# Optimization experiments

Measured on AMD Instinct MI355X. Metric: run time of the kernel, lower is better.

## Reference

```python
import jax, jax.numpy as jnp
import numpy as np

B, T, E, H = 2, 4096, 1024, 16
D = E // H  # head dim = 64

def setup_inputs() -> dict:
    key = jax.random.key(0)
    ks = jax.random.split(key, 5)
    x = jax.random.normal(ks[0], (B, T, E), dtype=jnp.float32)
    # torch Linear(n_embed, 3*n_embed): y = x @ W.T + b ; we store W already transposed as (E, 3E)
    w_qkv = jax.random.normal(ks[1], (E, 3 * E), dtype=jnp.float32) * (1.0 / np.sqrt(E))
    b_qkv = jax.random.normal(ks[2], (3 * E,), dtype=jnp.float32) * 0.02
    w_out = jax.random.normal(ks[3], (E, E), dtype=jnp.float32) * (1.0 / np.sqrt(E))
    b_out = jax.random.normal(ks[4], (E,), dtype=jnp.float32) * 0.02
    return {"x": x, "w_qkv": w_qkv, "b_qkv": b_qkv, "w_out": w_out, "b_out": b_out}

def reference(x, w_qkv, b_qkv, w_out, b_out):
    b, t, e = x.shape
    qkv = x @ w_qkv + b_qkv                      # (B,T,3E)
    # matches torch: view(B,T,H,3D) then chunk(3, dim=-1)
    qkv = qkv.reshape(b, t, H, 3 * D)
    q, k, v = jnp.split(qkv, 3, axis=-1)          # each (B,T,H,D)
    q = q.transpose(0, 2, 1, 3)                   # (B,H,T,D)
    k = k.transpose(0, 2, 1, 3)
    v = v.transpose(0, 2, 1, 3)
    scores = jnp.einsum('bhqd,bhkd->bhqk', q, k) / jnp.sqrt(jnp.float32(D))
    causal = jnp.tril(jnp.ones((t, t), dtype=bool))
    scores = jnp.where(causal, scores, jnp.float32(-jnp.inf))
    w = jax.nn.softmax(scores, axis=-1)           # (B,H,T,T)
    out = jnp.einsum('bhqk,bhkd->bhqd', w, v)     # (B,H,T,D)
    out = out.transpose(0, 2, 1, 3).reshape(b, t, e)
    return out @ w_out + b_out
```

## Files before the change

kernel.cpp:

```cpp
#include <hip/hip_runtime.h>
#include <stdint.h>
#include <math.h>

#define T_SEQ 4096

typedef __attribute__((ext_vector_type(8))) short short8;
typedef __attribute__((ext_vector_type(4))) float f32x4;
typedef __attribute__((ext_vector_type(16))) float f32x16;
typedef __attribute__((ext_vector_type(4))) uint16_t u16x4;

__device__ __forceinline__ uint16_t f2bf(float f) {
  uint32_t u = __float_as_uint(f);
  u += 0x7FFFu + ((u >> 16) & 1u);
  return (uint16_t)(u >> 16);
}

__device__ __forceinline__ void gload_lds16(const uint16_t* g, uint16_t* l) {
  __builtin_amdgcn_global_load_lds(
      (const __attribute__((address_space(1))) void*)g,
      (__attribute__((address_space(3))) void*)l, 16, 0, 0);
}

__global__ void __launch_bounds__(256) k_cvt(const float* __restrict__ in,
                                             uint16_t* __restrict__ out, int n4) {
  int i = blockIdx.x * 256 + threadIdx.x;
  if (i >= n4) return;
  float4 v = reinterpret_cast<const float4*>(in)[i];
  u16x4 o = { f2bf(v.x), f2bf(v.y), f2bf(v.z), f2bf(v.w) };
  reinterpret_cast<u16x4*>(out)[i] = o;
}

__global__ void __launch_bounds__(256) k_tc(const float* __restrict__ w,
                                            uint16_t* __restrict__ wt, int R, int C) {
  __shared__ uint16_t tile[32][33];
  int tx = threadIdx.x & 31, ty = threadIdx.x >> 5;
  int r0 = blockIdx.y * 32, c0 = blockIdx.x * 32;
#pragma unroll
  for (int i = 0; i < 4; i++)
    tile[ty + 8 * i][tx] = f2bf(w[(size_t)(r0 + ty + 8 * i) * C + c0 + tx]);
  __syncthreads();
#pragma unroll
  for (int i = 0; i < 4; i++)
    wt[(size_t)(c0 + ty + 8 * i) * R + r0 + tx] = tile[tx][ty + 8 * i];
}

__global__ void __launch_bounds__(256) k_vt(const uint16_t* __restrict__ qkv,
                                            uint16_t* __restrict__ vT) {
  __shared__ uint16_t tile[64][65];
  const int bh = blockIdx.y, b = bh >> 4, h = bh & 15;
  const int t0 = blockIdx.x * 64;
  const int tid = threadIdx.x;
  const int r = tid >> 3, c8 = tid & 7;
  const uint16_t* src = qkv + ((size_t)b * T_SEQ + t0) * 3072 + h * 192 + 128;
#pragma unroll
  for (int i = 0; i < 2; i++) {
    int row = r + 32 * i;
    short8 v = *reinterpret_cast<const short8*>(src + (size_t)row * 3072 + c8 * 8);
#pragma unroll
    for (int j = 0; j < 8; j++) tile[row][c8 * 8 + j] = (uint16_t)v[j];
  }
  __syncthreads();
  uint16_t* dst = vT + ((size_t)bh * 64) * T_SEQ + t0;
#pragma unroll
  for (int i = 0; i < 2; i++) {
    int d = r + 32 * i;
    short8 v;
#pragma unroll
    for (int j = 0; j < 8; j++) v[j] = (short)tile[c8 * 8 + j][d];
    *reinterpret_cast<short8*>(dst + (size_t)d * T_SEQ + c8 * 8) = v;
  }
}

template <int BF16_OUT>
__global__ void __launch_bounds__(256, 2) k_gemm(const uint16_t* __restrict__ A,
                                                 const uint16_t* __restrict__ BT,
                                                 const float* __restrict__ bias,
                                                 void* __restrict__ Cout,
                                                 int M, int N, int K) {
  __shared__ __align__(16) uint16_t As[2][128 * 64];
  __shared__ __align__(16) uint16_t Bs[2][128 * 64];
  const int tid = threadIdx.x;
  const int lane = tid & 63, wid = tid >> 6;
  const int lr = lane & 15, lg = lane >> 4;
  const int wr = wid >> 1, wc = wid & 1;

  const int bid = blockIdx.x;
  const int cpx = gridDim.x >> 3;
  const int lin = (bid & 7) * cpx + (bid >> 3);
  const int mt = M >> 7;
  const int n0 = (lin / mt) * 128;
  const int m0 = (lin % mt) * 128;

  const f32x4 vzero = {0.f, 0.f, 0.f, 0.f};
  f32x4 acc[4][4];
#pragma unroll
  for (int i = 0; i < 4; i++)
#pragma unroll
    for (int j = 0; j < 4; j++) acc[i][j] = vzero;

  const int sl = lane >> 3, ss = lane & 7;
  const int swzs = (ss ^ sl) * 8;
  const uint16_t* a0 = A + (size_t)(m0 + wid * 32 + sl) * K + swzs;
  const uint16_t* b0 = BT + (size_t)(n0 + wid * 32 + sl) * K + swzs;
  const size_t r8 = (size_t)8 * K;

#define STAGE(bsel, t)                                                   \
  do {                                                                   \
    const int koff_ = (t) * 64;                                          \
    gload_lds16(a0 + koff_,          &As[bsel][(wid * 32 + 0) * 64]);    \
    gload_lds16(a0 + r8 + koff_,     &As[bsel][(wid * 32 + 8) * 64]);    \
    gload_lds16(a0 + 2 * r8 + koff_, &As[bsel][(wid * 32 + 16) * 64]);   \
    gload_lds16(a0 + 3 * r8 + koff_, &As[bsel][(wid * 32 + 24) * 64]);   \
    gload_lds16(b0 + koff_,          &Bs[bsel][(wid * 32 + 0) * 64]);    \
    gload_lds16(b0 + r8 + koff_,     &Bs[bsel][(wid * 32 + 8) * 64]);    \
    gload_lds16(b0 + 2 * r8 + koff_, &Bs[bsel][(wid * 32 + 16) * 64]);   \
    gload_lds16(b0 + 3 * r8 + koff_, &Bs[bsel][(wid * 32 + 24) * 64]);   \
  } while (0)

  const int nt = K >> 6;
  const int fsw = lr & 7;
  STAGE(0, 0);
  STAGE(1, 1);
  __syncthreads();

  for (int t = 0; t < nt; ++t) {
    const int cur = t & 1;
#pragma unroll
    for (int ks = 0; ks < 2; ++ks) {
      const int col = (((ks * 4 + lg) ^ fsw) * 8);
      short8 af[4], bf[4];
#pragma unroll
      for (int mi = 0; mi < 4; ++mi)
        af[mi] = *reinterpret_cast<const short8*>(
            &As[cur][(wr * 64 + mi * 16 + lr) * 64 + col]);
#pragma unroll
      for (int nj = 0; nj < 4; ++nj)
        bf[nj] = *reinterpret_cast<const short8*>(
            &Bs[cur][(wc * 64 + nj * 16 + lr) * 64 + col]);
      __builtin_amdgcn_s_setprio(1);
#pragma unroll
      for (int mi = 0; mi < 4; ++mi)
#pragma unroll
        for (int nj = 0; nj < 4; ++nj)
          acc[mi][nj] = __builtin_amdgcn_mfma_f32_16x16x32_bf16(af[mi], bf[nj], acc[mi][nj], 0, 0, 0);
      __builtin_amdgcn_s_setprio(0);
    }
    __syncthreads();
    if (t + 2 < nt) STAGE(cur, t + 2);
  }
#undef STAGE

#pragma unroll
  for (int nj = 0; nj < 4; nj++) {
    int col = n0 + wc * 64 + nj * 16 + lr;
    float bv = bias[col];
#pragma unroll
    for (int mi = 0; mi < 4; mi++) {
      int rowb = m0 + wr * 64 + mi * 16 + lg * 4;
#pragma unroll
      for (int r = 0; r < 4; r++) {
        float v = acc[mi][nj][r] + bv;
        if (BF16_OUT)
          ((uint16_t*)Cout)[(size_t)(rowb + r) * N + col] = f2bf(v);
        else
          ((float*)Cout)[(size_t)(rowb + r) * N + col] = v;
      }
    }
  }
}

__global__ void __launch_bounds__(512, 2) k_gemm256(const uint16_t* __restrict__ A,
                                                    const uint16_t* __restrict__ BT,
                                                    const float* __restrict__ bias,
                                                    uint16_t* __restrict__ Cout,
                                                    int M, int N, int K) {
  __shared__ __align__(16) uint16_t As[2][256 * 32];
  __shared__ __align__(16) uint16_t Bs[2][256 * 32];
  const int tid = threadIdx.x;
  const int lane = tid & 63, wid = tid >> 6;
  const int lr = lane & 15, lg = lane >> 4;
  const int wr = wid >> 2, wc = wid & 3;

  const int bid = blockIdx.x;
  const int cpx = gridDim.x >> 3;
  const int lin = (bid & 7) * cpx + (bid >> 3);
  const int mt = M >> 8;
  const int n0 = (lin / mt) * 256;
  const int m0 = (lin % mt) * 256;

  const f32x4 vzero = {0.f, 0.f, 0.f, 0.f};
  f32x4 acc[8][4];
#pragma unroll
  for (int i = 0; i < 8; i++)
#pragma unroll
    for (int j = 0; j < 4; j++) acc[i][j] = vzero;

  const int row0 = tid >> 2;
  const int gc = (tid & 3) ^ ((tid >> 3) & 3);
  const uint16_t* a0 = A + (size_t)(m0 + row0) * K + gc * 8;
  const uint16_t* b0 = BT + (size_t)(n0 + row0) * K + gc * 8;
  const size_t rstep = (size_t)128 * K;

#define STAGE2(bsel, t)                                                    \
  do {                                                                     \
    const int ko_ = (t) * 32;                                              \
    gload_lds16(a0 + ko_,         &As[bsel][wid * 512]);                   \
    gload_lds16(a0 + rstep + ko_, &As[bsel][wid * 512 + 4096]);            \
    gload_lds16(b0 + ko_,         &Bs[bsel][wid * 512]);                   \
    gload_lds16(b0 + rstep + ko_, &Bs[bsel][wid * 512 + 4096]);            \
  } while (0)

  const int nt = K >> 5;
  const int fc = (lg ^ ((lr >> 1) & 3)) * 8;
  STAGE2(0, 0);
  STAGE2(1, 1);
  __syncthreads();

  for (int t = 0; t < nt; ++t) {
    const int cur = t & 1;
    short8 af[8], bf[4];
#pragma unroll
    for (int mi = 0; mi < 8; ++mi)
      af[mi] = *reinterpret_cast<const short8*>(
          &As[cur][(wr * 128 + mi * 16 + lr) * 32 + fc]);
#pragma unroll
    for (int nj = 0; nj < 4; ++nj)
      bf[nj] = *reinterpret_cast<const short8*>(
          &Bs[cur][(wc * 64 + nj * 16 + lr) * 32 + fc]);
    __builtin_amdgcn_s_setprio(1);
#pragma unroll
    for (int mi = 0; mi < 8; ++mi)
#pragma unroll
      for (int nj = 0; nj < 4; ++nj)
        acc[mi][nj] = __builtin_amdgcn_mfma_f32_16x16x32_bf16(af[mi], bf[nj], acc[mi][nj], 0, 0, 0);
    __builtin_amdgcn_s_setprio(0);
    __syncthreads();
    if (t + 2 < nt) STAGE2(cur, t + 2);
  }
#undef STAGE2

#pragma unroll
  for (int nj = 0; nj < 4; nj++) {
    int col = n0 + wc * 64 + nj * 16 + lr;
    float bv = bias[col];
#pragma unroll
    for (int mi = 0; mi < 8; mi++) {
      int rowb = m0 + wr * 128 + mi * 16 + lg * 4;
#pragma unroll
      for (int r = 0; r < 4; r++)
        Cout[(size_t)(rowb + r) * N + col] = f2bf(acc[mi][nj][r] + bv);
    }
  }
}

#define KVB 64
__global__ void __launch_bounds__(256) k_attn(const uint16_t* __restrict__ qkv,
                                              const uint16_t* __restrict__ vT,
                                              uint16_t* __restrict__ out) {
  __shared__ __align__(16) char lds[32768];
  const int tid = threadIdx.x;
  const int lane = tid & 63, wid = tid >> 6;
  const int l31 = lane & 31, hi = lane >> 5;
  const int hi4 = hi * 4;

  const int bid = blockIdx.x;
  const int xcd = bid & 7, j = bid >> 3;
  const int bh = xcd * 4 + (j & 3);
  const int qt = 31 - (j >> 2);
  const int b = bh >> 4, h = bh & 15;
  const int q0 = qt * 128;
  const size_t rowbase = (size_t)b * T_SEQ;
  const int hoff = h * 192;
  const uint16_t* Kg = qkv + rowbase * 3072 + hoff + 64;
  const uint16_t* Vg = vT + (size_t)bh * 64 * T_SEQ;

  const int sr = tid >> 3, sc = tid & 7;
  const int wsw = (sc ^ (sr & 7)) * 16;
  const float C_SC = 0.180336881f;

  int rslot[4];
#pragma unroll
  for (int c = 0; c < 4; c++) rslot[c] = (((2 * c + hi) ^ (lane & 7)) << 4);
  const int rowb128 = l31 * 128;

  const int qrow = q0 + wid * 32 + l31;
  short8 qf[4];
#pragma unroll
  for (int ks = 0; ks < 4; ks++) {
    short8 raw = *reinterpret_cast<const short8*>(
        qkv + (rowbase + qrow) * 3072 + hoff + hi * 8 + ks * 16);
    union { short8 s; uint32_t u[4]; } pk;
#pragma unroll
    for (int e = 0; e < 4; e++) {
      float f0 = __uint_as_float(((uint32_t)(uint16_t)raw[2 * e]) << 16) * C_SC;
      float f1 = __uint_as_float(((uint32_t)(uint16_t)raw[2 * e + 1]) << 16) * C_SC;
      asm("v_cvt_pk_bf16_f32 %0, %1, %2" : "=v"(pk.u[e]) : "v"(f0), "v"(f1));
    }
    qf[ks] = pk.s;
  }

  f32x16 o0, o1, zero16;
#pragma unroll
  for (int i = 0; i < 16; i++) zero16[i] = 0.f;
  o0 = zero16; o1 = zero16;
  float lpart = 0.f;

  const int nkt = 2 * qt + 2;
  const int qwmax = q0 + wid * 32 + 31;

  short8 rk0, rk1, rv0, rv1;
  rk0 = *reinterpret_cast<const short8*>(Kg + (size_t)sr * 3072 + sc * 8);
  rk1 = *reinterpret_cast<const short8*>(Kg + (size_t)(sr + 32) * 3072 + sc * 8);
  rv0 = *reinterpret_cast<const short8*>(Vg + (size_t)sr * T_SEQ + sc * 8);
  rv1 = *reinterpret_cast<const short8*>(Vg + (size_t)(sr + 32) * T_SEQ + sc * 8);
  {
    char* kb0 = lds;
    char* vb0 = lds + 16384;
    *reinterpret_cast<short8*>(kb0 + sr * 128 + wsw) = rk0;
    *reinterpret_cast<short8*>(kb0 + (sr + 32) * 128 + wsw) = rk1;
    *reinterpret_cast<short8*>(vb0 + sr * 128 + wsw) = rv0;
    *reinterpret_cast<short8*>(vb0 + (sr + 32) * 128 + wsw) = rv1;
  }
  if (nkt > 1) {
    rk0 = *reinterpret_cast<const short8*>(Kg + (size_t)(KVB + sr) * 3072 + sc * 8);
    rk1 = *reinterpret_cast<const short8*>(Kg + (size_t)(KVB + sr + 32) * 3072 + sc * 8);
    rv0 = *reinterpret_cast<const short8*>(Vg + (size_t)sr * T_SEQ + KVB + sc * 8);
    rv1 = *reinterpret_cast<const short8*>(Vg + (size_t)(sr + 32) * T_SEQ + KVB + sc * 8);
  }

  for (int kt = 0; kt < nkt; kt++) {
    __syncthreads();
    if (kt + 1 < nkt) {
      const int nsel = (kt + 1) & 1;
      char* kb = lds + (nsel ? 8192 : 0);
      char* vb = lds + 16384 + (nsel ? 8192 : 0);
      *reinterpret_cast<short8*>(kb + sr * 128 + wsw) = rk0;
      *reinterpret_cast<short8*>(kb + (sr + 32) * 128 + wsw) = rk1;
      *reinterpret_cast<short8*>(vb + sr * 128 + wsw) = rv0;
      *reinterpret_cast<short8*>(vb + (sr + 32) * 128 + wsw) = rv1;
      if (kt + 2 < nkt) {
        int k0n = (kt + 2) * KVB;
        rk0 = *reinterpret_cast<const short8*>(Kg + (size_t)(k0n + sr) * 3072 + sc * 8);
        rk1 = *reinterpret_cast<const short8*>(Kg + (size_t)(k0n + sr + 32) * 3072 + sc * 8);
        rv0 = *reinterpret_cast<const short8*>(Vg + (size_t)sr * T_SEQ + k0n + sc * 8);
        rv1 = *reinterpret_cast<const short8*>(Vg + (size_t)(sr + 32) * T_SEQ + k0n + sc * 8);
      }
    }

    if (kt * KVB <= qwmax) {
      const int csel = kt & 1;
      char* kcur = lds + (csel ? 8192 : 0);
      char* vcur = lds + 16384 + (csel ? 8192 : 0);
      const int ktb = kt * KVB;
      const bool notfull = (ktb + 63 > q0 + wid * 32);

      f32x16 s0 = zero16, s1 = zero16;
      __builtin_amdgcn_s_setprio(1);
#pragma unroll
      for (int ks = 0; ks < 4; ks++) {
        short8 kf0 = *reinterpret_cast<const short8*>(kcur + rowb128 + rslot[ks]);
        short8 kf1 = *reinterpret_cast<const short8*>(kcur + 4096 + rowb128 + rslot[ks]);
        s0 = __builtin_amdgcn_mfma_f32_32x32x16_bf16(kf0, qf[ks], s0, 0, 0, 0);
        s1 = __builtin_amdgcn_mfma_f32_32x32x16_bf16(kf1, qf[ks], s1, 0, 0, 0);
      }
      __builtin_amdgcn_s_setprio(0);

      uint32_t u0[8], u1[8];
#define SMAX_KB(SV, KB, U)                                                    \
  do {                                                                        \
    _Pragma("unroll")                                                         \
    for (int r = 0; r < 16; r++) {                                            \
      float v = SV[r];                                                        \
      if (notfull) {                                                          \
        int key = ktb + (KB) * 32 + (r & 3) + 8 * (r >> 2) + hi4;             \
        if (key > qrow) v = -INFINITY;                                        \
      }                                                                       \
      float p = __builtin_amdgcn_exp2f(v);                                    \
      SV[r] = p;                                                              \
      lpart += p;                                                             \
    }                                                                         \
    _Pragma("unroll")                                                         \
    for (int jj = 0; jj < 8; jj++)                                            \
      asm("v_cvt_pk_bf16_f32 %0, %1, %2"                                      \
          : "=v"(U[jj]) : "v"(SV[2 * jj]), "v"(SV[2 * jj + 1]));              \
    asm volatile("v_permlane32_swap_b32 %0, %1" : "+v"(U[0]), "+v"(U[2]));    \
    asm volatile("v_permlane32_swap_b32 %0, %1" : "+v"(U[1]), "+v"(U[3]));    \
    asm volatile("v_permlane32_swap_b32 %0, %1" : "+v"(U[4]), "+v"(U[6]));    \
    asm volatile("v_permlane32_swap_b32 %0, %1" : "+v"(U[5]), "+v"(U[7]));    \
  } while (0)

      SMAX_KB(s0, 0, u0);
      SMAX_KB(s1, 1, u1);
#undef SMAX_KB

      union { uint32_t u[4]; short8 s; } pf;
      __builtin_amdgcn_s_setprio(1);
#pragma unroll
      for (int kv = 0; kv < 4; kv++) {
        if (kv == 0) { pf.u[0] = u0[0]; pf.u[1] = u0[1]; pf.u[2] = u0[2]; pf.u[3] = u0[3]; }
        else if (kv == 1) { pf.u[0] = u0[4]; pf.u[1] = u0[5]; pf.u[2] = u0[6]; pf.u[3] = u0[7]; }
        else if (kv == 2) { pf.u[0] = u1[0]; pf.u[1] = u1[1]; pf.u[2] = u1[2]; pf.u[3] = u1[3]; }
        else { pf.u[0] = u1[4]; pf.u[1] = u1[5]; pf.u[2] = u1[6]; pf.u[3] = u1[7]; }
        short8 vf0 = *reinterpret_cast<const short8*>(vcur + rowb128 + rslot[kv]);
        short8 vf1 = *reinterpret_cast<const short8*>(vcur + 4096 + rowb128 + rslot[kv]);
        o0 = __builtin_amdgcn_mfma_f32_32x32x16_bf16(vf0, pf.s, o0, 0, 0, 0);
        o1 = __builtin_amdgcn_mfma_f32_32x32x16_bf16(vf1, pf.s, o1, 0, 0, 0);
      }
      __builtin_amdgcn_s_setprio(0);
    }
  }

  __syncthreads();
  float ltot = lpart + __shfl_xor(lpart, 32);
  float inv = 1.0f / ltot;
  char* scrb = lds + wid * 8192;
#pragma unroll
  for (int g = 0; g < 4; g++) {
    f32x4 w0, w1;
#pragma unroll
    for (int e = 0; e < 4; e++) { w0[e] = o0[4 * g + e] * inv; w1[e] = o1[4 * g + e] * inv; }
    int s0i = 2 * g + hi, s1i = s0i + 8;
    *reinterpret_cast<f32x4*>(scrb + l31 * 256 + ((s0i ^ (l31 & 7)) << 4)) = w0;
    *reinterpret_cast<f32x4*>(scrb + l31 * 256 + ((s1i ^ (l31 & 7)) << 4)) = w1;
  }
  asm volatile("s_waitcnt lgkmcnt(0)" ::: "memory");
  __builtin_amdgcn_sched_barrier(0);
  {
    int row = lane >> 1, half = lane & 1;
    uint16_t tmp[32];
#pragma unroll
    for (int k = 0; k < 8; k++) {
      f32x4 vv = *reinterpret_cast<const f32x4*>(
          scrb + row * 256 + (((half * 8 + k) ^ (row & 7)) << 4));
#pragma unroll
      for (int e = 0; e < 4; e++) tmp[k * 4 + e] = f2bf(vv[e]);
    }
    uint16_t* op = out + (rowbase + q0 + wid * 32 + row) * 1024 + h * 64 + half * 32;
#pragma unroll
    for (int k = 0; k < 4; k++)
      *reinterpret_cast<short8*>(op + k * 8) = *reinterpret_cast<const short8*>(tmp + k * 8);
  }
}

extern "C" void kernel_launch(void* const* d_in, const int* in_sizes, int n_in,
                              void* d_out, int out_size, void* d_ws, size_t ws_size,
                              hipStream_t stream) {
  const float* x = (const float*)d_in[0];
  const float* w_qkv = (const float*)d_in[1];
  const float* b_qkv = (const float*)d_in[2];
  const float* w_out = (const float*)d_in[3];
  const float* b_out = (const float*)d_in[4];
  float* out = (float*)d_out;

  uint8_t* ws = (uint8_t*)d_ws;
  uint16_t* x_bf  = (uint16_t*)(ws);
  uint16_t* wqkvT = (uint16_t*)(ws + (16u << 20));
  uint16_t* woutT = (uint16_t*)(ws + (22u << 20));
  uint16_t* qkv   = (uint16_t*)(ws + (24u << 20));
  uint16_t* vTbuf = (uint16_t*)(ws + (72u << 20));
  uint16_t* attn_o = x_bf;

  k_cvt<<<8192, 256, 0, stream>>>(x, x_bf, 2097152);
  k_tc<<<dim3(96, 32), 256, 0, stream>>>(w_qkv, wqkvT, 1024, 3072);
  k_tc<<<dim3(32, 32), 256, 0, stream>>>(w_out, woutT, 1024, 1024);
  k_gemm256<<<384, 512, 0, stream>>>(x_bf, wqkvT, b_qkv, qkv, 8192, 3072, 1024);
  k_vt<<<dim3(64, 32), 256, 0, stream>>>(qkv, vTbuf);
  k_attn<<<1024, 256, 0, stream>>>(qkv, vTbuf, attn_o);
  k_gemm<0><<<512, 256, 0, stream>>>(attn_o, woutT, b_out, out, 8192, 1024, 1024);
}
```

Measured before the change: 242.7 us.

## Deepen QKV GEMM K-tile to 64 and interleave async loads with MFMA phases

The QKV projection GEMM now uses a 64-wide K tile with a double buffer, twice the LDS per block, so occupancy drops to one block per CU. The global-to-LDS loads for the next tile are issued inside the MFMA phases, A before the first phase and B after it, instead of after the barrier. A new XOR swizzle over eight 16-byte chunks is meant to avoid LDS bank conflicts, and the wider tile halves the number of barriers per K step. The aim is to hide load latency behind MFMA work, at the cost of less occupancy and more live registers for the fragments.

```diff
diff --git a/kernel.cpp b/kernel.cpp
--- a/kernel.cpp
+++ b/kernel.cpp
@@ -169,13 +169,13 @@
   }
 }
 
-__global__ void __launch_bounds__(512, 2) k_gemm256(const uint16_t* __restrict__ A,
-                                                    const uint16_t* __restrict__ BT,
-                                                    const float* __restrict__ bias,
-                                                    uint16_t* __restrict__ Cout,
-                                                    int M, int N, int K) {
-  __shared__ __align__(16) uint16_t As[2][256 * 32];
-  __shared__ __align__(16) uint16_t Bs[2][256 * 32];
+__global__ void __launch_bounds__(512, 1) k_gemm256p(const uint16_t* __restrict__ A,
+                                                     const uint16_t* __restrict__ BT,
+                                                     const float* __restrict__ bias,
+                                                     uint16_t* __restrict__ Cout,
+                                                     int M, int N, int K) {
+  __shared__ __align__(16) uint16_t As[2][256 * 64];
+  __shared__ __align__(16) uint16_t Bs[2][256 * 64];
   const int tid = threadIdx.x;
   const int lane = tid & 63, wid = tid >> 6;
   const int lr = lane & 15, lg = lane >> 4;
@@ -195,49 +195,80 @@
 #pragma unroll
     for (int j = 0; j < 4; j++) acc[i][j] = vzero;
 
-  const int row0 = tid >> 2;
-  const int gc = (tid & 3) ^ ((tid >> 3) & 3);
-  const uint16_t* a0 = A + (size_t)(m0 + row0) * K + gc * 8;
-  const uint16_t* b0 = BT + (size_t)(n0 + row0) * K + gc * 8;
-  const size_t rstep = (size_t)128 * K;
-
-#define STAGE2(bsel, t)                                                    \
-  do {                                                                     \
-    const int ko_ = (t) * 32;                                              \
-    gload_lds16(a0 + ko_,         &As[bsel][wid * 512]);                   \
-    gload_lds16(a0 + rstep + ko_, &As[bsel][wid * 512 + 4096]);            \
-    gload_lds16(b0 + ko_,         &Bs[bsel][wid * 512]);                   \
-    gload_lds16(b0 + rstep + ko_, &Bs[bsel][wid * 512 + 4096]);            \
+  const int sl = lane >> 3, ss = lane & 7;
+  const int swzs = (ss ^ sl) * 8;
+  const uint16_t* a0 = A + (size_t)(m0 + wid * 32 + sl) * K + swzs;
+  const uint16_t* b0 = BT + (size_t)(n0 + wid * 32 + sl) * K + swzs;
+  const size_t r8 = (size_t)8 * K;
+
+#define STAGE_A(bsel, t)                                                  \
+  do {                                                                    \
+    const int ko_ = (t) * 64;                                             \
+    gload_lds16(a0 + ko_,          &As[bsel][(wid * 32 + 0) * 64]);       \
+    gload_lds16(a0 + r8 + ko_,     &As[bsel][(wid * 32 + 8) * 64]);       \
+    gload_lds16(a0 + 2 * r8 + ko_, &As[bsel][(wid * 32 + 16) * 64]);      \
+    gload_lds16(a0 + 3 * r8 + ko_, &As[bsel][(wid * 32 + 24) * 64]);      \
   } while (0)
-
-  const int nt = K >> 5;
-  const int fc = (lg ^ ((lr >> 1) & 3)) * 8;
-  STAGE2(0, 0);
-  STAGE2(1, 1);
+#define STAGE_B(bsel, t)                                                  \
+  do {                                                                    \
+    const int ko_ = (t) * 64;                                             \
+    gload_lds16(b0 + ko_,          &Bs[bsel][(wid * 32 + 0) * 64]);       \
+    gload_lds16(b0 + r8 + ko_,     &Bs[bsel][(wid * 32 + 8) * 64]);       \
+    gload_lds16(b0 + 2 * r8 + ko_, &Bs[bsel][(wid * 32 + 16) * 64]);      \
+    gload_lds16(b0 + 3 * r8 + ko_, &Bs[bsel][(wid * 32 + 24) * 64]);      \
+  } while (0)
+
+  const int nt = K >> 6;
+  const int fsw = lr & 7;
+  STAGE_A(0, 0);
+  STAGE_B(0, 0);
   __syncthreads();
 
   for (int t = 0; t < nt; ++t) {
     const int cur = t & 1;
-    short8 af[8], bf[4];
-#pragma unroll
-    for (int mi = 0; mi < 8; ++mi)
-      af[mi] = *reinterpret_cast<const short8*>(
-          &As[cur][(wr * 128 + mi * 16 + lr) * 32 + fc]);
+    const int nxt = cur ^ 1;
+
+    short8 bf[4][2];
 #pragma unroll
     for (int nj = 0; nj < 4; ++nj)
-      bf[nj] = *reinterpret_cast<const short8*>(
-          &Bs[cur][(wc * 64 + nj * 16 + lr) * 32 + fc]);
-    __builtin_amdgcn_s_setprio(1);
-#pragma unroll
-    for (int mi = 0; mi < 8; ++mi)
-#pragma unroll
-      for (int nj = 0; nj < 4; ++nj)
-        acc[mi][nj] = __builtin_amdgcn_mfma_f32_16x16x32_bf16(af[mi], bf[nj], acc[mi][nj], 0, 0, 0);
-    __builtin_amdgcn_s_setprio(0);
+#pragma unroll
+      for (int ks = 0; ks < 2; ++ks)
+        bf[nj][ks] = *reinterpret_cast<const short8*>(
+            &Bs[cur][(wc * 64 + nj * 16 + lr) * 64 + (((ks * 4 + lg) ^ fsw) * 8)]);
+
+#define PHASE(mi0)                                                            \
+  do {                                                                        \
+    short8 af0k0 = *reinterpret_cast<const short8*>(                          \
+        &As[cur][(wr * 128 + (mi0) * 16 + lr) * 64 + (((0 * 4 + lg) ^ fsw) * 8)]); \
+    short8 af0k1 = *reinterpret_cast<const short8*>(                          \
+        &As[cur][(wr * 128 + (mi0) * 16 + lr) * 64 + (((1 * 4 + lg) ^ fsw) * 8)]); \
+    short8 af1k0 = *reinterpret_cast<const short8*>(                          \
+        &As[cur][(wr * 128 + (mi0 + 1) * 16 + lr) * 64 + (((0 * 4 + lg) ^ fsw) * 8)]); \
+    short8 af1k1 = *reinterpret_cast<const short8*>(                          \
+        &As[cur][(wr * 128 + (mi0 + 1) * 16 + lr) * 64 + (((1 * 4 + lg) ^ fsw) * 8)]); \
+    __builtin_amdgcn_s_setprio(1);                                            \
+    _Pragma("unroll")                                                         \
+    for (int nj = 0; nj < 4; ++nj) {                                          \
+      acc[mi0][nj] = __builtin_amdgcn_mfma_f32_16x16x32_bf16(af0k0, bf[nj][0], acc[mi0][nj], 0, 0, 0); \
+      acc[mi0][nj] = __builtin_amdgcn_mfma_f32_16x16x32_bf16(af0k1, bf[nj][1], acc[mi0][nj], 0, 0, 0); \
+      acc[mi0 + 1][nj] = __builtin_amdgcn_mfma_f32_16x16x32_bf16(af1k0, bf[nj][0], acc[mi0 + 1][nj], 0, 0, 0); \
+      acc[mi0 + 1][nj] = __builtin_amdgcn_mfma_f32_16x16x32_bf16(af1k1, bf[nj][1], acc[mi0 + 1][nj], 0, 0, 0); \
+    }                                                                         \
+    __builtin_amdgcn_s_setprio(0);                                            \
+  } while (0)
+
+    if (t + 1 < nt) STAGE_A(nxt, t + 1);
+    PHASE(0);
+    if (t + 1 < nt) STAGE_B(nxt, t + 1);
+    PHASE(2);
+    PHASE(4);
+    PHASE(6);
+#undef PHASE
+
     __syncthreads();
-    if (t + 2 < nt) STAGE2(cur, t + 2);
-  }
-#undef STAGE2
+  }
+#undef STAGE_A
+#undef STAGE_B
 
 #pragma unroll
   for (int nj = 0; nj < 4; nj++) {
@@ -463,7 +494,7 @@
   k_cvt<<<8192, 256, 0, stream>>>(x, x_bf, 2097152);
   k_tc<<<dim3(96, 32), 256, 0, stream>>>(w_qkv, wqkvT, 1024, 3072);
   k_tc<<<dim3(32, 32), 256, 0, stream>>>(w_out, woutT, 1024, 1024);
-  k_gemm256<<<384, 512, 0, stream>>>(x_bf, wqkvT, b_qkv, qkv, 8192, 3072, 1024);
+  k_gemm256p<<<384, 512, 0, stream>>>(x_bf, wqkvT, b_qkv, qkv, 8192, 3072, 1024);
   k_vt<<<dim3(64, 32), 256, 0, stream>>>(qkv, vTbuf);
   k_attn<<<1024, 256, 0, stream>>>(qkv, vTbuf, attn_o);
   k_gemm<0><<<512, 256, 0, stream>>>(attn_o, woutT, b_out, out, 8192, 1024, 1024);
```

After: 220.3 us (median of 2 runs). 1.1x faster.
